# Kernel optimization log

Hardware: AMD Instinct MI355X
Metric: run time of the kernel (lower is better)

## Reference

```python
import jax, jax.numpy as jnp
import numpy as np

N = 50000      # nodes
E = 1600000    # edges
IN_DIM = 64
H = 8          # num_heads
D = 8          # out_dim per head


def setup_inputs() -> dict:
    key = jax.random.key(0)
    ks = jax.random.split(key, 12)
    scale = 1.0 / np.sqrt(IN_DIM)
    inp = {
        "h": jax.random.normal(ks[0], (N, IN_DIM), jnp.float32),
        "e": jax.random.normal(ks[1], (E, IN_DIM), jnp.float32),
        "Wq": jax.random.normal(ks[2], (IN_DIM, H * D), jnp.float32) * scale,
        "bq": jnp.zeros((H * D,), jnp.float32),
        "Wk": jax.random.normal(ks[3], (IN_DIM, H * D), jnp.float32) * scale,
        "bk": jnp.zeros((H * D,), jnp.float32),
        "Wv": jax.random.normal(ks[4], (IN_DIM, H * D), jnp.float32) * scale,
        "bv": jnp.zeros((H * D,), jnp.float32),
        "We": jax.random.normal(ks[5], (IN_DIM, H * D), jnp.float32) * scale,
        "be": jnp.zeros((H * D,), jnp.float32),
        "src": jax.random.randint(ks[6], (E,), 0, N, jnp.int32),
        "dst": jax.random.randint(ks[7], (E,), 0, N, jnp.int32),
    }
    return inp


def reference(h, e, Wq, bq, Wk, bk, Wv, bv, We, be, src, dst):
    n = h.shape[0]
    # Node projections -> [N, H, D]; edge projection -> [E, H, D]
    Q = (h @ Wq + bq).reshape(n, H, D)
    K = (h @ Wk + bk).reshape(n, H, D)
    V = (h @ Wv + bv).reshape(n, H, D)
    pe = (e @ We + be).reshape(-1, H, D)

    inv_sqrt_d = jnp.float32(1.0 / np.sqrt(D))
    # edge-wise: K[src] * Q[dst] / sqrt(D) * proj_e
    score = K[src] * Q[dst] * inv_sqrt_d * pe          # [E, H, D]
    e_out = score                                       # edge output (pre-exp)
    # clamped exp of per-head sum -> [E, H, 1]
    s = jnp.exp(jnp.clip(jnp.sum(score, axis=-1, keepdims=True), -5.0, 5.0))

    # aggregate to destination nodes (DGL recv side)
    wV = jax.ops.segment_sum(V[src] * s, dst, num_segments=n)   # [N, H, D]
    z = jax.ops.segment_sum(s, dst, num_segments=n)             # [N, H, 1]
    h_out = wV / (z + jnp.float32(1e-6))
    return h_out, e_out
```

## Files before the change

kernel.cpp:

```cpp
#include <hip/hip_runtime.h>


using short8 = __attribute__((ext_vector_type(8))) short;
using f32x16 = __attribute__((ext_vector_type(16))) float;

__device__ __forceinline__ short f2bf(float f) {
    unsigned u = __builtin_bit_cast(unsigned, f);
    u += 0x7FFF + ((u >> 16) & 1);
    return (short)(u >> 16);
}

__global__ __launch_bounds__(256)
void proj_kernel(const float* __restrict__ hsrc,
                 const float* __restrict__ Wq, const float* __restrict__ bq,
                 const float* __restrict__ Wk, const float* __restrict__ bk,
                 const float* __restrict__ Wv, const float* __restrict__ bv,
                 float* __restrict__ Q, float* __restrict__ K, float* __restrict__ V,
                 int n)
{
    const float* W;
    const float* b;
    float* out;
    if (blockIdx.y == 0)      { W = Wq; b = bq; out = Q; }
    else if (blockIdx.y == 1) { W = Wk; b = bk; out = K; }
    else                      { W = Wv; b = bv; out = V; }

    const int t    = threadIdx.x;
    const int lane = t & 63;
    const int w    = t >> 6;

    float wcol[64];
#pragma unroll
    for (int k = 0; k < 64; ++k) wcol[k] = W[k * 64 + lane];
    const float bias = b[lane];

    __shared__ float4 sh[16][16];
    const float4* __restrict__ h4 = (const float4*)hsrc;

    const int ngroups = (n + 15) >> 4;
    for (int g = blockIdx.x; g < ngroups; g += gridDim.x) {
        const int base = g << 4;
        {
            const int rs = t >> 4, c4 = t & 15;
            float4 v = make_float4(0.f, 0.f, 0.f, 0.f);
            if (base + rs < n) v = h4[(size_t)(base + rs) * 16 + c4];
            __syncthreads();
            sh[rs][c4] = v;
            __syncthreads();
        }
        float acc0 = bias, acc1 = bias, acc2 = bias, acc3 = bias;
#pragma unroll
        for (int k4 = 0; k4 < 16; ++k4) {
            const float w0 = wcol[k4 * 4 + 0], w1 = wcol[k4 * 4 + 1];
            const float w2 = wcol[k4 * 4 + 2], w3 = wcol[k4 * 4 + 3];
            const float4 a = sh[w * 4 + 0][k4];
            const float4 bb = sh[w * 4 + 1][k4];
            const float4 c = sh[w * 4 + 2][k4];
            const float4 d = sh[w * 4 + 3][k4];
            acc0 = fmaf(a.w,  w3, fmaf(a.z,  w2, fmaf(a.y,  w1, fmaf(a.x,  w0, acc0))));
            acc1 = fmaf(bb.w, w3, fmaf(bb.z, w2, fmaf(bb.y, w1, fmaf(bb.x, w0, acc1))));
            acc2 = fmaf(c.w,  w3, fmaf(c.z,  w2, fmaf(c.y,  w1, fmaf(c.x,  w0, acc2))));
            acc3 = fmaf(d.w,  w3, fmaf(d.z,  w2, fmaf(d.y,  w1, fmaf(d.x,  w0, acc3))));
        }
        const int n0 = base + w * 4;
        if (n0 + 0 < n) out[(size_t)(n0 + 0) * 64 + lane] = acc0;
        if (n0 + 1 < n) out[(size_t)(n0 + 1) * 64 + lane] = acc1;
        if (n0 + 2 < n) out[(size_t)(n0 + 2) * 64 + lane] = acc2;
        if (n0 + 3 < n) out[(size_t)(n0 + 3) * 64 + lane] = acc3;
    }
}

__global__ __launch_bounds__(256)
void rank_kernel(const int* __restrict__ dst, int* __restrict__ counts,
                 int* __restrict__ rank, int E)
{
    int i = blockIdx.x * 256 + threadIdx.x;
    const int stride = gridDim.x * 256;
    for (; i < E; i += stride) {
        rank[i] = atomicAdd(&counts[dst[i]], 1);
    }
}

__global__ __launch_bounds__(1024)
void scan1_kernel(const int* __restrict__ counts, int* __restrict__ offsets,
                  int* __restrict__ bsum, int n)
{
    const int t = threadIdx.x;
    const int lane = t & 63;
    const int w = t >> 6;
    __shared__ int wsum[16];
    const int i = blockIdx.x * 1024 + t;
    const int v = (i < n) ? counts[i] : 0;
    int x = v;
#pragma unroll
    for (int d = 1; d < 64; d <<= 1) {
        int y = __shfl_up(x, d);
        if (lane >= d) x += y;
    }
    if (lane == 63) wsum[w] = x;
    __syncthreads();
    if (w == 0 && lane < 16) {
        int s = wsum[lane];
#pragma unroll
        for (int d = 1; d < 16; d <<= 1) {
            int y = __shfl_up(s, d);
            if (lane >= d) s += y;
        }
        wsum[lane] = s;
    }
    __syncthreads();
    const int excl = ((w == 0) ? 0 : wsum[w - 1]) + (x - v);
    if (i < n) offsets[i] = excl;
    if (t == 1023) bsum[blockIdx.x] = excl + v;
}

__global__ __launch_bounds__(64)
void scan2_kernel(int* __restrict__ bsum, int nb)
{
    const int lane = threadIdx.x;
    const int v = (lane < nb) ? bsum[lane] : 0;
    int x = v;
#pragma unroll
    for (int d = 1; d < 64; d <<= 1) {
        int y = __shfl_up(x, d);
        if (lane >= d) x += y;
    }
    if (lane < nb) bsum[lane] = x - v;
}

__global__ __launch_bounds__(1024)
void scan3_kernel(int* __restrict__ offsets, const int* __restrict__ bsum,
                  int n, int E)
{
    const int i = blockIdx.x * 1024 + threadIdx.x;
    if (i < n) offsets[i] += bsum[blockIdx.x];
    if (blockIdx.x == 0 && threadIdx.x == 0) offsets[n] = E;
}

__global__ __launch_bounds__(256)
void edge_kernel(const float* __restrict__ e,
                 const float* __restrict__ We, const float* __restrict__ be,
                 const int* __restrict__ src, const int* __restrict__ dst,
                 const float* __restrict__ Q, const float* __restrict__ K,
                 float* __restrict__ e_out, float* __restrict__ sg, int E)
{
    __shared__ float4 tile4[4][32 * 8];
    const int t    = threadIdx.x;
    const int lane = t & 63;
    const int wu   = __builtin_amdgcn_readfirstlane(t >> 6);
    const int lid  = lane & 31;
    const int hi   = lane >> 5;
    float4* const myT4 = tile4[wu];
    const float inv = 0.35355339059327373f;

    short8 Afr[2][4];
#pragma unroll
    for (int jh = 0; jh < 2; ++jh)
#pragma unroll
        for (int ks = 0; ks < 4; ++ks)
#pragma unroll
            for (int g = 0; g < 2; ++g)
#pragma unroll
                for (int i = 0; i < 4; ++i)
                    Afr[jh][ks][4 * g + i] =
                        f2bf(We[(16 * ks + 8 * g + 4 * hi + i) * 64 + 32 * jh + lid]);

    const int ntiles = (E + 63) >> 6;
    for (int tb = blockIdx.x * 4 + wu; tb < ntiles; tb += gridDim.x * 4) {
        const int base = tb << 6;

#pragma unroll
        for (int eh = 0; eh < 2; ++eh) {
            const int erow_i = base + eh * 32 + lid;
            const int erc = erow_i < E ? erow_i : (E - 1);
            const int se = src[erc];
            const int de = dst[erc];

            const float* er = e + (size_t)erc * 64 + 4 * hi;
            short8 Bfr[4];
#pragma unroll
            for (int ks = 0; ks < 4; ++ks) {
                const float4 p0 = *(const float4*)(er + 16 * ks);
                const float4 p1 = *(const float4*)(er + 16 * ks + 8);
                Bfr[ks][0] = f2bf(p0.x); Bfr[ks][1] = f2bf(p0.y);
                Bfr[ks][2] = f2bf(p0.z); Bfr[ks][3] = f2bf(p0.w);
                Bfr[ks][4] = f2bf(p1.x); Bfr[ks][5] = f2bf(p1.y);
                Bfr[ks][6] = f2bf(p1.z); Bfr[ks][7] = f2bf(p1.w);
            }

            float gate[8];
#pragma unroll
            for (int jh = 0; jh < 2; ++jh) {
                f32x16 D = {};
#pragma unroll
                for (int ks = 0; ks < 4; ++ks)
                    D = __builtin_amdgcn_mfma_f32_32x32x16_bf16(
                            Afr[jh][ks], Bfr[ks], D, 0, 0, 0);

                asm volatile("s_waitcnt lgkmcnt(0)" ::: "memory");

                const float* kb = K + (size_t)se * 64 + 32 * jh + 4 * hi;
                const float* qb = Q + (size_t)de * 64 + 32 * jh + 4 * hi;
#pragma unroll
                for (int hd = 0; hd < 4; ++hd) {
                    const float4 kv  = *(const float4*)(kb + 8 * hd);
                    const float4 qv  = *(const float4*)(qb + 8 * hd);
                    const float4 bev = *(const float4*)(be + 32 * jh + 8 * hd + 4 * hi);
                    const float s0 = kv.x * qv.x * inv * (D[4 * hd + 0] + bev.x);
                    const float s1 = kv.y * qv.y * inv * (D[4 * hd + 1] + bev.y);
                    const float s2 = kv.z * qv.z * inv * (D[4 * hd + 2] + bev.z);
                    const float s3 = kv.w * qv.w * inv * (D[4 * hd + 3] + bev.w);
                    const int c4 = (2 * hd + hi) ^ (lid & 7);
                    myT4[lid * 8 + c4] = make_float4(s0, s1, s2, s3);
                    float p = (s0 + s1) + (s2 + s3);
                    const float full = p + __shfl_xor(p, 32);
                    gate[jh * 4 + hd] = expf(fminf(fmaxf(full, -5.f), 5.f));
                }

                const int r8 = lane >> 3, m = lane & 7;
#pragma unroll
                for (int it = 0; it < 4; ++it) {
                    const int row = it * 8 + r8;
                    const int edge2 = base + eh * 32 + row;
                    const float4 v = myT4[row * 8 + (m ^ (row & 7))];
                    if (edge2 < E)
                        *((float4*)e_out + (size_t)edge2 * 16 + jh * 8 + m) = v;
                }
            }

            if (erow_i < E) {
                const float4 g = (hi == 0)
                    ? make_float4(gate[0], gate[1], gate[2], gate[3])
                    : make_float4(gate[4], gate[5], gate[6], gate[7]);
                *(float4*)(sg + (size_t)erow_i * 8 + hi * 4) = g;
            }
        }
    }
}

__global__ __launch_bounds__(256)
void reorder_kernel(const float* __restrict__ sg, const int* __restrict__ src,
                    const int* __restrict__ dst, const int* __restrict__ rank,
                    const int* __restrict__ offs,
                    float* __restrict__ s_sorted, int* __restrict__ src_sorted,
                    int E)
{
    int i = blockIdx.x * 256 + threadIdx.x;
    const int stride = gridDim.x * 256;
    for (; i < E; i += stride) {
        const int rk = offs[dst[i]] + rank[i];
        const float4 g0 = *(const float4*)(sg + (size_t)i * 8);
        const float4 g1 = *(const float4*)(sg + (size_t)i * 8 + 4);
        *(float4*)(s_sorted + (size_t)rk * 8)     = g0;
        *(float4*)(s_sorted + (size_t)rk * 8 + 4) = g1;
        src_sorted[rk] = src[i];
    }
}

__global__ __launch_bounds__(256)
void aggregate_kernel(const int* __restrict__ offsets,
                      const int* __restrict__ src_sorted,
                      const float* __restrict__ s_sorted,
                      const float* __restrict__ V,
                      float* __restrict__ hout, int n)
{
    const int w = (blockIdx.x * 256 + threadIdx.x) >> 6;
    const int lane = threadIdx.x & 63;
    if (w >= n) return;
    const int o0 = offsets[w], o1 = offsets[w + 1];
    const int head = lane >> 3;
    float acc = 0.f, zacc = 0.f;
    int j = o0;
    for (; j + 4 <= o1; j += 4) {
        const int sv0 = src_sorted[j + 0];
        const int sv1 = src_sorted[j + 1];
        const int sv2 = src_sorted[j + 2];
        const int sv3 = src_sorted[j + 3];
        const float s0 = s_sorted[(size_t)(j + 0) * 8 + head];
        const float s1 = s_sorted[(size_t)(j + 1) * 8 + head];
        const float s2 = s_sorted[(size_t)(j + 2) * 8 + head];
        const float s3 = s_sorted[(size_t)(j + 3) * 8 + head];
        const float v0 = V[(size_t)sv0 * 64 + lane];
        const float v1 = V[(size_t)sv1 * 64 + lane];
        const float v2 = V[(size_t)sv2 * 64 + lane];
        const float v3 = V[(size_t)sv3 * 64 + lane];
        acc = fmaf(v0, s0, acc);
        acc = fmaf(v1, s1, acc);
        acc = fmaf(v2, s2, acc);
        acc = fmaf(v3, s3, acc);
        zacc += (s0 + s1) + (s2 + s3);
    }
    for (; j < o1; ++j) {
        const int sv = src_sorted[j];
        const float s = s_sorted[(size_t)j * 8 + head];
        acc = fmaf(V[(size_t)sv * 64 + lane], s, acc);
        zacc += s;
    }
    hout[(size_t)w * 64 + lane] = acc / (zacc + 1e-6f);
}

extern "C" void kernel_launch(void* const* d_in, const int* in_sizes, int n_in,
                              void* d_out, int out_size, void* d_ws, size_t ws_size,
                              hipStream_t stream)
{
    const float* h  = (const float*)d_in[0];
    const float* e  = (const float*)d_in[1];
    const float* Wq = (const float*)d_in[2];
    const float* bq = (const float*)d_in[3];
    const float* Wk = (const float*)d_in[4];
    const float* bk = (const float*)d_in[5];
    const float* Wv = (const float*)d_in[6];
    const float* bv = (const float*)d_in[7];
    const float* We = (const float*)d_in[8];
    const float* be = (const float*)d_in[9];
    const int* src  = (const int*)d_in[10];
    const int* dst  = (const int*)d_in[11];

    const int N = in_sizes[0] / 64;
    const int E = in_sizes[1] / 64;

    float* hout  = (float*)d_out;
    float* e_out = (float*)d_out + (size_t)N * 64;

    char* ws = (char*)d_ws;
    float* Q = (float*)ws;                 ws += (size_t)N * 64 * sizeof(float);
    float* K = (float*)ws;                 ws += (size_t)N * 64 * sizeof(float);
    float* V = (float*)ws;                 ws += (size_t)N * 64 * sizeof(float);
    float* sg = (float*)ws;                ws += (size_t)E * 8 * sizeof(float);
    float* s_sorted = (float*)ws;          ws += (size_t)E * 8 * sizeof(float);
    int* src_sorted = (int*)ws;            ws += (size_t)E * sizeof(int);
    int* rank = (int*)ws;                  ws += (size_t)E * sizeof(int);
    int* counts  = (int*)ws;               ws += (size_t)N * sizeof(int);
    int* offsets = (int*)ws;               ws += (size_t)(N + 1) * sizeof(int);
    int* bsum    = (int*)ws;               ws += 64 * sizeof(int);

    hipMemsetAsync(counts, 0, (size_t)N * sizeof(int), stream);

    proj_kernel<<<dim3(512, 3), dim3(256), 0, stream>>>(
        h, Wq, bq, Wk, bk, Wv, bv, Q, K, V, N);

    rank_kernel<<<dim3(2048), dim3(256), 0, stream>>>(dst, counts, rank, E);

    const int nb = (N + 1023) / 1024;
    scan1_kernel<<<dim3(nb), dim3(1024), 0, stream>>>(counts, offsets, bsum, N);
    scan2_kernel<<<dim3(1), dim3(64), 0, stream>>>(bsum, nb);
    scan3_kernel<<<dim3(nb), dim3(1024), 0, stream>>>(offsets, bsum, N, E);

    const int ntiles = (E + 63) >> 6;
    const int eblocks = (ntiles + 3) / 4;
    edge_kernel<<<dim3(eblocks), dim3(256), 0, stream>>>(
        e, We, be, src, dst, Q, K, e_out, sg, E);

    reorder_kernel<<<dim3(2048), dim3(256), 0, stream>>>(
        sg, src, dst, rank, offsets, s_sorted, src_sorted, E);

    const int ablocks = (N * 64 + 255) / 256;
    aggregate_kernel<<<dim3(ablocks), dim3(256), 0, stream>>>(
        offsets, src_sorted, s_sorted, V, hout, N);
}
```

Measured before the change: 580.3 us.

## Fuse rank into projection launch, hoist edge gathers, widen aggregate unroll

Merges the rank/atomic-count kernel into the projection kernel as a fourth grid row, so both run in one launch and overlap. The edge kernel now issues all e-row, K and Q gathers at the start of the tile, before the MFMAs, to raise memory-level parallelism. The aggregate loop unrolls to 8 neighbors with loads batched ahead of the FMAs. The cost is higher register pressure, which may lower occupancy, and the rank grid is smaller (512 blocks instead of 2048).

```diff
diff --git a/kernel.cpp b/kernel.cpp
--- a/kernel.cpp
+++ b/kernel.cpp
@@ -11,13 +11,23 @@
 }
 
 __global__ __launch_bounds__(256)
-void proj_kernel(const float* __restrict__ hsrc,
-                 const float* __restrict__ Wq, const float* __restrict__ bq,
-                 const float* __restrict__ Wk, const float* __restrict__ bk,
-                 const float* __restrict__ Wv, const float* __restrict__ bv,
-                 float* __restrict__ Q, float* __restrict__ K, float* __restrict__ V,
-                 int n)
-{
+void proj_rank_kernel(const float* __restrict__ hsrc,
+                      const float* __restrict__ Wq, const float* __restrict__ bq,
+                      const float* __restrict__ Wk, const float* __restrict__ bk,
+                      const float* __restrict__ Wv, const float* __restrict__ bv,
+                      float* __restrict__ Q, float* __restrict__ K, float* __restrict__ V,
+                      const int* __restrict__ dst, int* __restrict__ counts,
+                      int* __restrict__ rank, int n, int E)
+{
+    if (blockIdx.y == 3) {
+        int i = blockIdx.x * 256 + threadIdx.x;
+        const int stride = gridDim.x * 256;
+        for (; i < E; i += stride) {
+            rank[i] = atomicAdd(&counts[dst[i]], 1);
+        }
+        return;
+    }
+
     const float* W;
     const float* b;
     float* out;
@@ -70,17 +80,6 @@
     }
 }
 
-__global__ __launch_bounds__(256)
-void rank_kernel(const int* __restrict__ dst, int* __restrict__ counts,
-                 int* __restrict__ rank, int E)
-{
-    int i = blockIdx.x * 256 + threadIdx.x;
-    const int stride = gridDim.x * 256;
-    for (; i < E; i += stride) {
-        rank[i] = atomicAdd(&counts[dst[i]], 1);
-    }
-}
-
 __global__ __launch_bounds__(1024)
 void scan1_kernel(const int* __restrict__ counts, int* __restrict__ offsets,
                   int* __restrict__ bsum, int n)
@@ -177,15 +176,31 @@
             const int de = dst[erc];
 
             const float* er = e + (size_t)erc * 64 + 4 * hi;
+            float4 p0 = *(const float4*)(er + 0),  p1 = *(const float4*)(er + 8);
+            float4 p2 = *(const float4*)(er + 16), p3 = *(const float4*)(er + 24);
+            float4 p4 = *(const float4*)(er + 32), p5 = *(const float4*)(er + 40);
+            float4 p6 = *(const float4*)(er + 48), p7 = *(const float4*)(er + 56);
+
+            const float* kb = K + (size_t)se * 64 + 4 * hi;
+            const float* qb = Q + (size_t)de * 64 + 4 * hi;
+            float4 kv[2][4], qv[2][4];
+#pragma unroll
+            for (int jh = 0; jh < 2; ++jh)
+#pragma unroll
+                for (int hd = 0; hd < 4; ++hd) {
+                    kv[jh][hd] = *(const float4*)(kb + 32 * jh + 8 * hd);
+                    qv[jh][hd] = *(const float4*)(qb + 32 * jh + 8 * hd);
+                }
+
             short8 Bfr[4];
 #pragma unroll
             for (int ks = 0; ks < 4; ++ks) {
-                const float4 p0 = *(const float4*)(er + 16 * ks);
-                const float4 p1 = *(const float4*)(er + 16 * ks + 8);
-                Bfr[ks][0] = f2bf(p0.x); Bfr[ks][1] = f2bf(p0.y);
-                Bfr[ks][2] = f2bf(p0.z); Bfr[ks][3] = f2bf(p0.w);
-                Bfr[ks][4] = f2bf(p1.x); Bfr[ks][5] = f2bf(p1.y);
-                Bfr[ks][6] = f2bf(p1.z); Bfr[ks][7] = f2bf(p1.w);
+                const float4 pa = (ks == 0) ? p0 : (ks == 1) ? p2 : (ks == 2) ? p4 : p6;
+                const float4 pb = (ks == 0) ? p1 : (ks == 1) ? p3 : (ks == 2) ? p5 : p7;
+                Bfr[ks][0] = f2bf(pa.x); Bfr[ks][1] = f2bf(pa.y);
+                Bfr[ks][2] = f2bf(pa.z); Bfr[ks][3] = f2bf(pa.w);
+                Bfr[ks][4] = f2bf(pb.x); Bfr[ks][5] = f2bf(pb.y);
+                Bfr[ks][6] = f2bf(pb.z); Bfr[ks][7] = f2bf(pb.w);
             }
 
             float gate[8];
@@ -199,21 +214,19 @@
 
                 asm volatile("s_waitcnt lgkmcnt(0)" ::: "memory");
 
-                const float* kb = K + (size_t)se * 64 + 32 * jh + 4 * hi;
-                const float* qb = Q + (size_t)de * 64 + 32 * jh + 4 * hi;
 #pragma unroll
                 for (int hd = 0; hd < 4; ++hd) {
-                    const float4 kv  = *(const float4*)(kb + 8 * hd);
-                    const float4 qv  = *(const float4*)(qb + 8 * hd);
                     const float4 bev = *(const float4*)(be + 32 * jh + 8 * hd + 4 * hi);
-                    const float s0 = kv.x * qv.x * inv * (D[4 * hd + 0] + bev.x);
-                    const float s1 = kv.y * qv.y * inv * (D[4 * hd + 1] + bev.y);
-                    const float s2 = kv.z * qv.z * inv * (D[4 * hd + 2] + bev.z);
-                    const float s3 = kv.w * qv.w * inv * (D[4 * hd + 3] + bev.w);
+                    const float4 k4 = kv[jh][hd];
+                    const float4 q4 = qv[jh][hd];
+                    const float s0 = k4.x * q4.x * inv * (D[4 * hd + 0] + bev.x);
+                    const float s1 = k4.y * q4.y * inv * (D[4 * hd + 1] + bev.y);
+                    const float s2 = k4.z * q4.z * inv * (D[4 * hd + 2] + bev.z);
+                    const float s3 = k4.w * q4.w * inv * (D[4 * hd + 3] + bev.w);
                     const int c4 = (2 * hd + hi) ^ (lid & 7);
                     myT4[lid * 8 + c4] = make_float4(s0, s1, s2, s3);
-                    float p = (s0 + s1) + (s2 + s3);
-                    const float full = p + __shfl_xor(p, 32);
+                    float pp = (s0 + s1) + (s2 + s3);
+                    const float full = pp + __shfl_xor(pp, 32);
                     gate[jh * 4 + hd] = expf(fminf(fmaxf(full, -5.f), 5.f));
                 }
 
@@ -271,24 +284,23 @@
     const int head = lane >> 3;
     float acc = 0.f, zacc = 0.f;
     int j = o0;
-    for (; j + 4 <= o1; j += 4) {
-        const int sv0 = src_sorted[j + 0];
-        const int sv1 = src_sorted[j + 1];
-        const int sv2 = src_sorted[j + 2];
-        const int sv3 = src_sorted[j + 3];
-        const float s0 = s_sorted[(size_t)(j + 0) * 8 + head];
-        const float s1 = s_sorted[(size_t)(j + 1) * 8 + head];
-        const float s2 = s_sorted[(size_t)(j + 2) * 8 + head];
-        const float s3 = s_sorted[(size_t)(j + 3) * 8 + head];
-        const float v0 = V[(size_t)sv0 * 64 + lane];
-        const float v1 = V[(size_t)sv1 * 64 + lane];
-        const float v2 = V[(size_t)sv2 * 64 + lane];
-        const float v3 = V[(size_t)sv3 * 64 + lane];
-        acc = fmaf(v0, s0, acc);
-        acc = fmaf(v1, s1, acc);
-        acc = fmaf(v2, s2, acc);
-        acc = fmaf(v3, s3, acc);
-        zacc += (s0 + s1) + (s2 + s3);
+    for (; j + 8 <= o1; j += 8) {
+        int   sv[8];
+        float ss[8];
+#pragma unroll
+        for (int q = 0; q < 8; ++q) {
+            sv[q] = src_sorted[j + q];
+            ss[q] = s_sorted[(size_t)(j + q) * 8 + head];
+        }
+        float vv[8];
+#pragma unroll
+        for (int q = 0; q < 8; ++q)
+            vv[q] = V[(size_t)sv[q] * 64 + lane];
+#pragma unroll
+        for (int q = 0; q < 8; ++q) {
+            acc = fmaf(vv[q], ss[q], acc);
+            zacc += ss[q];
+        }
     }
     for (; j < o1; ++j) {
         const int sv = src_sorted[j];
@@ -336,10 +348,8 @@
 
     hipMemsetAsync(counts, 0, (size_t)N * sizeof(int), stream);
 
-    proj_kernel<<<dim3(512, 3), dim3(256), 0, stream>>>(
-        h, Wq, bq, Wk, bk, Wv, bv, Q, K, V, N);
-
-    rank_kernel<<<dim3(2048), dim3(256), 0, stream>>>(dst, counts, rank, E);
+    proj_rank_kernel<<<dim3(512, 4), dim3(256), 0, stream>>>(
+        h, Wq, bq, Wk, bk, Wv, bv, Q, K, V, dst, counts, rank, N, E);
 
     const int nb = (N + 1023) / 1024;
     scan1_kernel<<<dim3(nb), dim3(1024), 0, stream>>>(counts, offsets, bsum, N);
```

New measurement: 565.9 us. -2.5%, faster.
